# Kernel tuning notes

Hardware: AMD Instinct MI355X
Metric: run time of the kernel (lower is better)

Reference implementation:

```python
import jax, jax.numpy as jnp
import numpy as np

B, S, H = 2, 2048, 2048
E = 16          # num_experts
K = 8           # num_experts_per_tok
I = 1408        # moe_intermediate_size


def setup_inputs() -> dict:
    key = jax.random.key(0)
    k1, k2, k3, k4 = jax.random.split(key, 4)
    hidden_states = jax.random.normal(k1, (B, S, H), dtype=jnp.float32)
    router_w = jax.random.normal(k2, (H, E), dtype=jnp.float32) * 0.02
    gate_up = jax.random.normal(k3, (E, H, 2 * I), dtype=jnp.float32) * 0.02
    down = jax.random.normal(k4, (E, I, H), dtype=jnp.float32) * 0.02
    return {"hidden_states": hidden_states, "router_w": router_w,
            "gate_up": gate_up, "down": down, "top_k": K}


def reference(hidden_states, router_w, gate_up, down, top_k):
    b, s, h = hidden_states.shape
    x = hidden_states.reshape(-1, h)                      # [T, H]
    logits = x @ router_w                                 # [T, E]
    probs = jax.nn.softmax(logits, axis=-1)               # stable softmax
    topk_vals, _topk_idx = jax.lax.top_k(probs, top_k)    # [T, K]
    routing_weights = topk_vals / jnp.sum(topk_vals, axis=-1, keepdims=True)

    # Faithful to nki_fused_moe_kernel: expert k in 0..top_k-1 uses weights[k]
    # (the kernel indexes gate_up_weights[k], not the selected expert index).
    inter = down.shape[1]
    gu = jnp.einsum('th,khd->tkd', x, gate_up[:top_k])    # [T, K, 2I]
    gate = gu[..., :inter]
    up = gu[..., inter:]
    hid = jax.nn.silu(gate) * up                          # SwiGLU, [T, K, I]
    expert_out = jnp.einsum('tki,kih->tkh', hid, down[:top_k])  # [T, K, H]
    out = jnp.sum(expert_out * routing_weights[..., None], axis=1)  # [T, H]
    return out.reshape(b, s, h), routing_weights
```

## Files before the change

### kernel.cpp

```cpp
#include <hip/hip_runtime.h>
#include <hip/hip_bf16.h>

#define T_TOK 4096
#define H_DIM 2048
#define I_DIM 1408
#define KEXP 8
#define E_TOT 16
#define KDIM2 (KEXP * I_DIM)

typedef __attribute__((ext_vector_type(8))) short short8;
typedef __attribute__((ext_vector_type(4))) float floatx4;

__device__ __forceinline__ unsigned short f2bf(float f) {
  unsigned int u = __builtin_bit_cast(unsigned int, f);
  u += 0x7fffu + ((u >> 16) & 1u);
  return (unsigned short)(u >> 16);
}

#define GLD16(gp, lp) \
  __builtin_amdgcn_global_load_lds((const __attribute__((address_space(1))) unsigned int*)(gp), \
                                   (__attribute__((address_space(3))) unsigned int*)(lp), 16, 0, 0)

__global__ __launch_bounds__(256) void k_convert_x(const float* __restrict__ in,
                                                   unsigned short* __restrict__ out, int n4) {
  int i = blockIdx.x * 256 + threadIdx.x;
  if (i >= n4) return;
  floatx4 v = ((const floatx4*)in)[i];
  union { unsigned short s[4]; unsigned long long u; } o;
  o.s[0] = f2bf(v.x); o.s[1] = f2bf(v.y); o.s[2] = f2bf(v.z); o.s[3] = f2bf(v.w);
  ((unsigned long long*)out)[i] = o.u;
}

__global__ __launch_bounds__(256) void k_transpose_bf(const float* __restrict__ in,
    unsigned short* __restrict__ out, int C, long inBatch, long outStride, long outBatch) {
  __shared__ unsigned short ldsT[32][68];
  const int tid = threadIdx.x;
  const int c = tid & 31;
  const int r8 = tid >> 5;
  const long zin = (long)blockIdx.z * inBatch;
  const int x0 = blockIdx.x * 32;
  const int y0 = blockIdx.y * 64;
  const float* ip = in + zin + (long)(y0 + r8) * C + x0 + c;
#pragma unroll
  for (int j = 0; j < 8; j++)
    ldsT[c][r8 + 8 * j] = f2bf(ip[(long)(8 * j) * C]);
  __syncthreads();
  const long zout = (long)blockIdx.z * outBatch;
#pragma unroll
  for (int p = 0; p < 2; p++) {
    int u = tid + 256 * p;
    int cc = u >> 4;
    int rg = u & 15;
    unsigned long long v = *(const unsigned long long*)&ldsT[cc][rg * 4];
    *(unsigned long long*)(out + (long)(x0 + cc) * outStride + zout + y0 + rg * 4) = v;
  }
}

__global__ __launch_bounds__(64) void k_router(const float* __restrict__ X,
    const float* __restrict__ Wr, float* __restrict__ rw_out, float* __restrict__ rw_ws) {
  const int t = blockIdx.x;
  const int lane = threadIdx.x;
  float acc[E_TOT];
#pragma unroll
  for (int e = 0; e < E_TOT; e++) acc[e] = 0.f;
  const float* xr = X + (size_t)t * H_DIM;
  for (int h = lane; h < H_DIM; h += 64) {
    float xv = xr[h];
    const float* w = Wr + (size_t)h * E_TOT;
#pragma unroll
    for (int e = 0; e < E_TOT; e++) acc[e] += xv * w[e];
  }
#pragma unroll
  for (int off = 32; off > 0; off >>= 1) {
#pragma unroll
    for (int e = 0; e < E_TOT; e++) acc[e] += __shfl_down(acc[e], off);
  }
  if (lane == 0) {
    float v[E_TOT];
#pragma unroll
    for (int e = 0; e < E_TOT; e++) v[e] = acc[e];
    float top[KEXP];
    for (int j = 0; j < KEXP; j++) {
      int bi = 0; float bv = v[0];
      for (int e = 1; e < E_TOT; e++) { if (v[e] > bv) { bv = v[e]; bi = e; } }
      top[j] = bv; v[bi] = -1e30f;
    }
    float m = top[0], s = 0.f, ex[KEXP];
    for (int j = 0; j < KEXP; j++) { ex[j] = __expf(top[j] - m); s += ex[j]; }
    float inv = 1.f / s;
    for (int j = 0; j < KEXP; j++) {
      float w = ex[j] * inv;
      rw_out[t * KEXP + j] = w;
      rw_ws[t * KEXP + j] = w;
    }
  }
}

__global__ __launch_bounds__(256, 2) void k_gemm1(
    const unsigned short* __restrict__ Xb, const unsigned short* __restrict__ GUT,
    const float* __restrict__ rw, unsigned short* __restrict__ hid) {
  __shared__ unsigned short lA[128 * 32];
  __shared__ unsigned short lG[64 * 32];
  __shared__ unsigned short lU[64 * 32];
  __shared__ float rwS[128];

  const int tid = threadIdx.x;
  const int lane = tid & 63;
  const int wid = tid >> 6;
  const int n0 = blockIdx.x * 64;
  const int m0 = blockIdx.y * 128;
  const int ke = blockIdx.z;

  if (tid < 128) rwS[tid] = rw[(m0 + tid) * KEXP + ke];

  const unsigned short* Gq = GUT + (size_t)ke * (2 * I_DIM * H_DIM) + (size_t)n0 * H_DIM;
  const unsigned short* Uq = Gq + (size_t)I_DIM * H_DIM;

  const int srow = tid >> 2;
  const int scol = (tid & 3) * 8;
  const unsigned short* pA  = Xb + (size_t)(m0 + srow) * H_DIM + scol;
  const unsigned short* pA2 = pA + (size_t)64 * H_DIM;
  const unsigned short* pG  = Gq + (size_t)srow * H_DIM + scol;
  const unsigned short* pU  = Uq + (size_t)srow * H_DIM + scol;
  unsigned short* dA  = lA + tid * 8;
  unsigned short* dA2 = lA + 2048 + tid * 8;
  unsigned short* dG  = lG + tid * 8;
  unsigned short* dU  = lU + tid * 8;

  floatx4 accg[4][2], accu[4][2];
  const floatx4 zero = {0.f, 0.f, 0.f, 0.f};
#pragma unroll
  for (int i = 0; i < 4; i++)
#pragma unroll
    for (int j = 0; j < 2; j++) { accg[i][j] = zero; accu[i][j] = zero; }

  const int wm = (wid >> 1) * 64;
  const int wn = (wid & 1) * 32;
  const int lr = lane & 15;
  const int lq = lane >> 4;

  for (int h0 = 0; h0 < H_DIM; h0 += 32) {
    GLD16(pA + h0, dA);
    GLD16(pA2 + h0, dA2);
    GLD16(pG + h0, dG);
    GLD16(pU + h0, dU);
    __syncthreads();
    short8 af[4], gf[2], uf[2];
#pragma unroll
    for (int mt = 0; mt < 4; mt++)
      af[mt] = *(const short8*)(lA + (wm + mt * 16 + lr) * 32 + lq * 8);
#pragma unroll
    for (int nt = 0; nt < 2; nt++) {
      gf[nt] = *(const short8*)(lG + (wn + nt * 16 + lr) * 32 + lq * 8);
      uf[nt] = *(const short8*)(lU + (wn + nt * 16 + lr) * 32 + lq * 8);
    }
#pragma unroll
    for (int mt = 0; mt < 4; mt++)
#pragma unroll
      for (int nt = 0; nt < 2; nt++) {
        accg[mt][nt] = __builtin_amdgcn_mfma_f32_16x16x32_bf16(af[mt], gf[nt], accg[mt][nt], 0, 0, 0);
        accu[mt][nt] = __builtin_amdgcn_mfma_f32_16x16x32_bf16(af[mt], uf[nt], accu[mt][nt], 0, 0, 0);
      }
    __syncthreads();
  }

#pragma unroll
  for (int mt = 0; mt < 4; mt++) {
#pragma unroll
    for (int nt = 0; nt < 2; nt++) {
#pragma unroll
      for (int r = 0; r < 4; r++) {
        int lrow = wm + mt * 16 + lq * 4 + r;
        int col = n0 + wn + nt * 16 + lr;
        float g = accg[mt][nt][r];
        float u = accu[mt][nt][r];
        float s = g / (1.f + __expf(-g));
        float hv = s * u * rwS[lrow];
        hid[(size_t)(m0 + lrow) * KDIM2 + ke * I_DIM + col] = f2bf(hv);
      }
    }
  }
}

__global__ __launch_bounds__(256, 2) void k_gemm2(
    const unsigned short* __restrict__ Ah, const unsigned short* __restrict__ Bt,
    float* __restrict__ part) {
  __shared__ unsigned short lA[128 * 32];
  __shared__ unsigned short lB[128 * 32];
  const int tid = threadIdx.x;
  const int lane = tid & 63;
  const int wid = tid >> 6;
  const int n0 = blockIdx.x * 128;
  const int m0 = blockIdx.y * 128;
  const int sz = blockIdx.z;
  const int kb   = (sz == 0) ? 0 : 3776 + (sz - 1) * 3744;
  const int kend = (sz == 0) ? 3776 : kb + 3744;
  float* out = part + (size_t)sz * T_TOK * H_DIM;

  const int srow = tid >> 2;
  const int scol = (tid & 3) * 8;
  const unsigned short* pA  = Ah + (size_t)(m0 + srow) * KDIM2 + scol;
  const unsigned short* pA2 = pA + (size_t)64 * KDIM2;
  const unsigned short* pB  = Bt + (size_t)(n0 + srow) * KDIM2 + scol;
  const unsigned short* pB2 = pB + (size_t)64 * KDIM2;
  unsigned short* dA  = lA + tid * 8;
  unsigned short* dA2 = lA + 2048 + tid * 8;
  unsigned short* dB  = lB + tid * 8;
  unsigned short* dB2 = lB + 2048 + tid * 8;

  floatx4 acc[4][4];
  const floatx4 zero = {0.f, 0.f, 0.f, 0.f};
#pragma unroll
  for (int i = 0; i < 4; i++)
#pragma unroll
    for (int j = 0; j < 4; j++) acc[i][j] = zero;

  const int wm = (wid >> 1) * 64;
  const int wn = (wid & 1) * 64;
  const int lr = lane & 15;
  const int lq = lane >> 4;

  for (int k0 = kb; k0 < kend; k0 += 32) {
    GLD16(pA + k0, dA);
    GLD16(pA2 + k0, dA2);
    GLD16(pB + k0, dB);
    GLD16(pB2 + k0, dB2);
    __syncthreads();
    short8 af[4], bfr[4];
#pragma unroll
    for (int mt = 0; mt < 4; mt++)
      af[mt] = *(const short8*)(lA + (wm + mt * 16 + lr) * 32 + lq * 8);
#pragma unroll
    for (int nt = 0; nt < 4; nt++)
      bfr[nt] = *(const short8*)(lB + (wn + nt * 16 + lr) * 32 + lq * 8);
#pragma unroll
    for (int mt = 0; mt < 4; mt++)
#pragma unroll
      for (int nt = 0; nt < 4; nt++)
        acc[mt][nt] = __builtin_amdgcn_mfma_f32_16x16x32_bf16(af[mt], bfr[nt], acc[mt][nt], 0, 0, 0);
    __syncthreads();
  }

#pragma unroll
  for (int mt = 0; mt < 4; mt++)
#pragma unroll
    for (int nt = 0; nt < 4; nt++)
#pragma unroll
      for (int r = 0; r < 4; r++)
        out[(size_t)(m0 + wm + mt * 16 + lq * 4 + r) * H_DIM + (n0 + wn + nt * 16 + lr)] =
            acc[mt][nt][r];
}

__global__ __launch_bounds__(256) void k_reduce3(const float* __restrict__ p,
                                                 float* __restrict__ out, int n4) {
  int i = blockIdx.x * 256 + threadIdx.x;
  if (i >= n4) return;
  const floatx4* p0 = (const floatx4*)p;
  const floatx4* p1 = p0 + (size_t)T_TOK * H_DIM / 4;
  const floatx4* p2 = p1 + (size_t)T_TOK * H_DIM / 4;
  floatx4 a = p0[i], b = p1[i], c = p2[i];
  floatx4 r = {a.x + b.x + c.x, a.y + b.y + c.y, a.z + b.z + c.z, a.w + b.w + c.w};
  ((floatx4*)out)[i] = r;
}

__global__ void k_ws_fail(float* out) {
  if (threadIdx.x == 0 && blockIdx.x == 0) out[0] = 1.0e6f;
}

extern "C" void kernel_launch(void* const* d_in, const int* in_sizes, int n_in,
                              void* d_out, int out_size, void* d_ws, size_t ws_size,
                              hipStream_t stream) {
  const float* X  = (const float*)d_in[0];
  const float* Wr = (const float*)d_in[1];
  const float* GU = (const float*)d_in[2];
  const float* DW = (const float*)d_in[3];
  float* out = (float*)d_out;
  float* rw_out = out + (size_t)T_TOK * H_DIM;

  const size_t oX   = 0;
  const size_t oGUT = oX   + (size_t)T_TOK * H_DIM * 2;
  const size_t oDT  = oGUT + (size_t)KEXP * 2 * I_DIM * H_DIM * 2;
  const size_t oHid = oDT  + (size_t)KEXP * I_DIM * H_DIM * 2;
  const size_t oRW  = oHid + (size_t)T_TOK * KDIM2 * 2;
  const size_t need = oRW  + (size_t)T_TOK * KEXP * 4;

  if (ws_size < need) {
    k_ws_fail<<<1, 64, 0, stream>>>(out);
    return;
  }

  unsigned short* Xb  = (unsigned short*)((char*)d_ws + oX);
  unsigned short* GUT = (unsigned short*)((char*)d_ws + oGUT);
  unsigned short* DT  = (unsigned short*)((char*)d_ws + oDT);
  unsigned short* Hid = (unsigned short*)((char*)d_ws + oHid);
  float* rwW = (float*)((char*)d_ws + oRW);
  float* Part = (float*)d_ws;

  k_convert_x<<<dim3((T_TOK * H_DIM / 4 + 255) / 256), 256, 0, stream>>>(X, Xb, T_TOK * H_DIM / 4);

  k_transpose_bf<<<dim3(2 * I_DIM / 32, H_DIM / 64, KEXP), 256, 0, stream>>>(
      GU, GUT, 2 * I_DIM, (long)H_DIM * 2 * I_DIM, (long)H_DIM, (long)2 * I_DIM * H_DIM);

  k_transpose_bf<<<dim3(H_DIM / 32, I_DIM / 64, KEXP), 256, 0, stream>>>(
      DW, DT, H_DIM, (long)I_DIM * H_DIM, (long)KDIM2, (long)I_DIM);

  k_router<<<dim3(T_TOK), 64, 0, stream>>>(X, Wr, rw_out, rwW);

  k_gemm1<<<dim3(I_DIM / 64, T_TOK / 128, KEXP), 256, 0, stream>>>(Xb, GUT, rwW, Hid);

  k_gemm2<<<dim3(H_DIM / 128, T_TOK / 128, 3), 256, 0, stream>>>(Hid, DT, Part);

  k_reduce3<<<dim3(T_TOK * H_DIM / 4 / 256), 256, 0, stream>>>(Part, out, T_TOK * H_DIM / 4);
}
```

Baseline: 1.446 ms.

## Double-buffer LDS in both GEMMs, swizzle LDS, remap blocks, drop split-K reduce

Both GEMM kernels now double-buffer their LDS tiles, so the global-to-LDS load for the next K step is issued before computing on the current one. They also apply an XOR swizzle to the LDS column layout to reduce bank conflicts. Block indices are remapped into a 1-D grid, interleaved by blockIdx modulo 8, to change how tiles are spread across XCDs for cache locality. The split-K of 3 in gemm2 and its reduce kernel are removed, so gemm2 writes straight to the output. That removes the partial-buffer traffic but leaves only 512 blocks, each with a longer K loop.

```diff
diff --git a/kernel.cpp b/kernel.cpp
--- a/kernel.cpp
+++ b/kernel.cpp
@@ -99,17 +99,21 @@
 __global__ __launch_bounds__(256, 2) void k_gemm1(
     const unsigned short* __restrict__ Xb, const unsigned short* __restrict__ GUT,
     const float* __restrict__ rw, unsigned short* __restrict__ hid) {
-  __shared__ unsigned short lA[128 * 32];
-  __shared__ unsigned short lG[64 * 32];
-  __shared__ unsigned short lU[64 * 32];
+  __shared__ unsigned short lA[2][128 * 32];
+  __shared__ unsigned short lG[2][64 * 32];
+  __shared__ unsigned short lU[2][64 * 32];
   __shared__ float rwS[128];
 
   const int tid = threadIdx.x;
   const int lane = tid & 63;
   const int wid = tid >> 6;
-  const int n0 = blockIdx.x * 64;
-  const int m0 = blockIdx.y * 128;
-  const int ke = blockIdx.z;
+
+  const int wg = (blockIdx.x & 7) * 704 + (blockIdx.x >> 3);
+  const int bx = wg % 22;
+  const int t1 = wg / 22;
+  const int n0 = bx * 64;
+  const int m0 = (t1 & 31) * 128;
+  const int ke = t1 >> 5;
 
   if (tid < 128) rwS[tid] = rw[(m0 + tid) * KEXP + ke];
 
@@ -117,15 +121,11 @@
   const unsigned short* Uq = Gq + (size_t)I_DIM * H_DIM;
 
   const int srow = tid >> 2;
-  const int scol = (tid & 3) * 8;
-  const unsigned short* pA  = Xb + (size_t)(m0 + srow) * H_DIM + scol;
+  const int scol8 = ((tid & 3) ^ ((tid >> 3) & 3)) * 8;
+  const unsigned short* pA  = Xb + (size_t)(m0 + srow) * H_DIM + scol8;
   const unsigned short* pA2 = pA + (size_t)64 * H_DIM;
-  const unsigned short* pG  = Gq + (size_t)srow * H_DIM + scol;
-  const unsigned short* pU  = Uq + (size_t)srow * H_DIM + scol;
-  unsigned short* dA  = lA + tid * 8;
-  unsigned short* dA2 = lA + 2048 + tid * 8;
-  unsigned short* dG  = lG + tid * 8;
-  unsigned short* dU  = lU + tid * 8;
+  const unsigned short* pG  = Gq + (size_t)srow * H_DIM + scol8;
+  const unsigned short* pU  = Uq + (size_t)srow * H_DIM + scol8;
 
   floatx4 accg[4][2], accu[4][2];
   const floatx4 zero = {0.f, 0.f, 0.f, 0.f};
@@ -138,31 +138,46 @@
   const int wn = (wid & 1) * 32;
   const int lr = lane & 15;
   const int lq = lane >> 4;
-
-  for (int h0 = 0; h0 < H_DIM; h0 += 32) {
-    GLD16(pA + h0, dA);
-    GLD16(pA2 + h0, dA2);
-    GLD16(pG + h0, dG);
-    GLD16(pU + h0, dU);
+  const int lsw8 = (lq ^ ((lr >> 1) & 3)) * 8;
+
+#define STAGE1(B, H0) do { \
+    GLD16(pA  + (H0), &lA[B][tid * 8]); \
+    GLD16(pA2 + (H0), &lA[B][2048 + tid * 8]); \
+    GLD16(pG  + (H0), &lG[B][tid * 8]); \
+    GLD16(pU  + (H0), &lU[B][tid * 8]); \
+  } while (0)
+
+#define COMP1(B) do { \
+    short8 af[4], gf[2], uf[2]; \
+    _Pragma("unroll") \
+    for (int mt = 0; mt < 4; mt++) \
+      af[mt] = *(const short8*)(&lA[B][(wm + mt * 16 + lr) * 32 + lsw8]); \
+    _Pragma("unroll") \
+    for (int nt = 0; nt < 2; nt++) { \
+      gf[nt] = *(const short8*)(&lG[B][(wn + nt * 16 + lr) * 32 + lsw8]); \
+      uf[nt] = *(const short8*)(&lU[B][(wn + nt * 16 + lr) * 32 + lsw8]); \
+    } \
+    _Pragma("unroll") \
+    for (int mt = 0; mt < 4; mt++) \
+      _Pragma("unroll") \
+      for (int nt = 0; nt < 2; nt++) { \
+        accg[mt][nt] = __builtin_amdgcn_mfma_f32_16x16x32_bf16(af[mt], gf[nt], accg[mt][nt], 0, 0, 0); \
+        accu[mt][nt] = __builtin_amdgcn_mfma_f32_16x16x32_bf16(af[mt], uf[nt], accu[mt][nt], 0, 0, 0); \
+      } \
+  } while (0)
+
+  STAGE1(0, 0);
+  __syncthreads();
+  for (int h0 = 0; h0 < H_DIM; h0 += 64) {
+    STAGE1(1, h0 + 32);
+    COMP1(0);
     __syncthreads();
-    short8 af[4], gf[2], uf[2];
-#pragma unroll
-    for (int mt = 0; mt < 4; mt++)
-      af[mt] = *(const short8*)(lA + (wm + mt * 16 + lr) * 32 + lq * 8);
-#pragma unroll
-    for (int nt = 0; nt < 2; nt++) {
-      gf[nt] = *(const short8*)(lG + (wn + nt * 16 + lr) * 32 + lq * 8);
-      uf[nt] = *(const short8*)(lU + (wn + nt * 16 + lr) * 32 + lq * 8);
-    }
-#pragma unroll
-    for (int mt = 0; mt < 4; mt++)
-#pragma unroll
-      for (int nt = 0; nt < 2; nt++) {
-        accg[mt][nt] = __builtin_amdgcn_mfma_f32_16x16x32_bf16(af[mt], gf[nt], accg[mt][nt], 0, 0, 0);
-        accu[mt][nt] = __builtin_amdgcn_mfma_f32_16x16x32_bf16(af[mt], uf[nt], accu[mt][nt], 0, 0, 0);
-      }
+    if (h0 + 64 < H_DIM) STAGE1(0, h0 + 64);
+    COMP1(1);
     __syncthreads();
   }
+#undef STAGE1
+#undef COMP1
 
 #pragma unroll
   for (int mt = 0; mt < 4; mt++) {
@@ -184,29 +199,23 @@
 
 __global__ __launch_bounds__(256, 2) void k_gemm2(
     const unsigned short* __restrict__ Ah, const unsigned short* __restrict__ Bt,
-    float* __restrict__ part) {
-  __shared__ unsigned short lA[128 * 32];
-  __shared__ unsigned short lB[128 * 32];
+    float* __restrict__ out) {
+  __shared__ unsigned short lA[2][128 * 32];
+  __shared__ unsigned short lB[2][128 * 32];
   const int tid = threadIdx.x;
   const int lane = tid & 63;
   const int wid = tid >> 6;
-  const int n0 = blockIdx.x * 128;
-  const int m0 = blockIdx.y * 128;
-  const int sz = blockIdx.z;
-  const int kb   = (sz == 0) ? 0 : 3776 + (sz - 1) * 3744;
-  const int kend = (sz == 0) ? 3776 : kb + 3744;
-  float* out = part + (size_t)sz * T_TOK * H_DIM;
+
+  const int wg = (blockIdx.x & 7) * 64 + (blockIdx.x >> 3);
+  const int n0 = (wg & 15) * 128;
+  const int m0 = (wg >> 4) * 128;
 
   const int srow = tid >> 2;
-  const int scol = (tid & 3) * 8;
-  const unsigned short* pA  = Ah + (size_t)(m0 + srow) * KDIM2 + scol;
+  const int scol8 = ((tid & 3) ^ ((tid >> 3) & 3)) * 8;
+  const unsigned short* pA  = Ah + (size_t)(m0 + srow) * KDIM2 + scol8;
   const unsigned short* pA2 = pA + (size_t)64 * KDIM2;
-  const unsigned short* pB  = Bt + (size_t)(n0 + srow) * KDIM2 + scol;
+  const unsigned short* pB  = Bt + (size_t)(n0 + srow) * KDIM2 + scol8;
   const unsigned short* pB2 = pB + (size_t)64 * KDIM2;
-  unsigned short* dA  = lA + tid * 8;
-  unsigned short* dA2 = lA + 2048 + tid * 8;
-  unsigned short* dB  = lB + tid * 8;
-  unsigned short* dB2 = lB + 2048 + tid * 8;
 
   floatx4 acc[4][4];
   const floatx4 zero = {0.f, 0.f, 0.f, 0.f};
@@ -219,27 +228,42 @@
   const int wn = (wid & 1) * 64;
   const int lr = lane & 15;
   const int lq = lane >> 4;
-
-  for (int k0 = kb; k0 < kend; k0 += 32) {
-    GLD16(pA + k0, dA);
-    GLD16(pA2 + k0, dA2);
-    GLD16(pB + k0, dB);
-    GLD16(pB2 + k0, dB2);
+  const int lsw8 = (lq ^ ((lr >> 1) & 3)) * 8;
+
+#define STAGE2(B, K0) do { \
+    GLD16(pA  + (K0), &lA[B][tid * 8]); \
+    GLD16(pA2 + (K0), &lA[B][2048 + tid * 8]); \
+    GLD16(pB  + (K0), &lB[B][tid * 8]); \
+    GLD16(pB2 + (K0), &lB[B][2048 + tid * 8]); \
+  } while (0)
+
+#define COMP2(B) do { \
+    short8 af[4], bfr[4]; \
+    _Pragma("unroll") \
+    for (int mt = 0; mt < 4; mt++) \
+      af[mt] = *(const short8*)(&lA[B][(wm + mt * 16 + lr) * 32 + lsw8]); \
+    _Pragma("unroll") \
+    for (int nt = 0; nt < 4; nt++) \
+      bfr[nt] = *(const short8*)(&lB[B][(wn + nt * 16 + lr) * 32 + lsw8]); \
+    _Pragma("unroll") \
+    for (int mt = 0; mt < 4; mt++) \
+      _Pragma("unroll") \
+      for (int nt = 0; nt < 4; nt++) \
+        acc[mt][nt] = __builtin_amdgcn_mfma_f32_16x16x32_bf16(af[mt], bfr[nt], acc[mt][nt], 0, 0, 0); \
+  } while (0)
+
+  STAGE2(0, 0);
+  __syncthreads();
+  for (int k0 = 0; k0 < KDIM2; k0 += 64) {
+    STAGE2(1, k0 + 32);
+    COMP2(0);
     __syncthreads();
-    short8 af[4], bfr[4];
-#pragma unroll
-    for (int mt = 0; mt < 4; mt++)
-      af[mt] = *(const short8*)(lA + (wm + mt * 16 + lr) * 32 + lq * 8);
-#pragma unroll
-    for (int nt = 0; nt < 4; nt++)
-      bfr[nt] = *(const short8*)(lB + (wn + nt * 16 + lr) * 32 + lq * 8);
-#pragma unroll
-    for (int mt = 0; mt < 4; mt++)
-#pragma unroll
-      for (int nt = 0; nt < 4; nt++)
-        acc[mt][nt] = __builtin_amdgcn_mfma_f32_16x16x32_bf16(af[mt], bfr[nt], acc[mt][nt], 0, 0, 0);
+    if (k0 + 64 < KDIM2) STAGE2(0, k0 + 64);
+    COMP2(1);
     __syncthreads();
   }
+#undef STAGE2
+#undef COMP2
 
 #pragma unroll
   for (int mt = 0; mt < 4; mt++)
@@ -249,18 +273,6 @@
       for (int r = 0; r < 4; r++)
         out[(size_t)(m0 + wm + mt * 16 + lq * 4 + r) * H_DIM + (n0 + wn + nt * 16 + lr)] =
             acc[mt][nt][r];
-}
-
-__global__ __launch_bounds__(256) void k_reduce3(const float* __restrict__ p,
-                                                 float* __restrict__ out, int n4) {
-  int i = blockIdx.x * 256 + threadIdx.x;
-  if (i >= n4) return;
-  const floatx4* p0 = (const floatx4*)p;
-  const floatx4* p1 = p0 + (size_t)T_TOK * H_DIM / 4;
-  const floatx4* p2 = p1 + (size_t)T_TOK * H_DIM / 4;
-  floatx4 a = p0[i], b = p1[i], c = p2[i];
-  floatx4 r = {a.x + b.x + c.x, a.y + b.y + c.y, a.z + b.z + c.z, a.w + b.w + c.w};
-  ((floatx4*)out)[i] = r;
 }
 
 __global__ void k_ws_fail(float* out) {
@@ -294,7 +306,6 @@
   unsigned short* DT  = (unsigned short*)((char*)d_ws + oDT);
   unsigned short* Hid = (unsigned short*)((char*)d_ws + oHid);
   float* rwW = (float*)((char*)d_ws + oRW);
-  float* Part = (float*)d_ws;
 
   k_convert_x<<<dim3((T_TOK * H_DIM / 4 + 255) / 256), 256, 0, stream>>>(X, Xb, T_TOK * H_DIM / 4);
 
@@ -306,9 +317,7 @@
 
   k_router<<<dim3(T_TOK), 64, 0, stream>>>(X, Wr, rw_out, rwW);
 
-  k_gemm1<<<dim3(I_DIM / 64, T_TOK / 128, KEXP), 256, 0, stream>>>(Xb, GUT, rwW, Hid);
-
-  k_gemm2<<<dim3(H_DIM / 128, T_TOK / 128, 3), 256, 0, stream>>>(Hid, DT, Part);
-
-  k_reduce3<<<dim3(T_TOK * H_DIM / 4 / 256), 256, 0, stream>>>(Part, out, T_TOK * H_DIM / 4);
-}
+  k_gemm1<<<dim3((I_DIM / 64) * (T_TOK / 128) * KEXP), 256, 0, stream>>>(Xb, GUT, rwW, Hid);
+
+  k_gemm2<<<dim3((H_DIM / 128) * (T_TOK / 128)), 256, 0, stream>>>(Hid, DT, out);
+}
```

New measurement: 1.334 ms. 1.08x faster.
